# Kernel tuning notes

Measured on AMD Instinct MI355X. Metric: run time of the kernel, lower is better.

The kernel has to match this reference:

```python
import jax, jax.numpy as jnp
import numpy as np

DIM = 256
NUM_HEADS = 8
HEAD_DIM = DIM // NUM_HEADS
SCALE = HEAD_DIM ** -0.5
KSIZE = 5


def setup_inputs() -> dict:
    key = jax.random.key(0)
    ks = jax.random.split(key, 6)
    B, C, H, W = 8, DIM, 32, 32
    x = jax.random.normal(ks[0], (B, C, H, W), dtype=jnp.float32)
    qkv_w = jax.random.normal(ks[1], (3 * C, C), dtype=jnp.float32) * 0.02  # 1x1 conv, no bias
    proj_w = jax.random.normal(ks[2], (C, C), dtype=jnp.float32) * 0.02    # 1x1 conv
    proj_b = jax.random.normal(ks[3], (C,), dtype=jnp.float32) * 0.02
    lepe_w = jax.random.normal(ks[4], (C, 1, KSIZE, KSIZE), dtype=jnp.float32) * 0.02  # depthwise
    lepe_b = jax.random.normal(ks[5], (C,), dtype=jnp.float32) * 0.02
    return {"x": x, "qkv_w": qkv_w, "proj_w": proj_w, "proj_b": proj_b,
            "lepe_w": lepe_w, "lepe_b": lepe_b}


def _forward(x, qkv_w, proj_w, proj_b, lepe_w, lepe_b):
    B, C, H, W = x.shape
    N = H * W
    # 1x1 conv qkv: [B,3C,H,W]
    qkv = jnp.einsum('bchw,oc->bohw', x, qkv_w)
    q, k, v = jnp.split(qkv, 3, axis=1)
    # reshape to [B, heads, head_dim, N]
    qh = q.reshape(B, NUM_HEADS, HEAD_DIM, N)
    kh = k.reshape(B, NUM_HEADS, HEAD_DIM, N)
    vh = v.reshape(B, NUM_HEADS, HEAD_DIM, N)
    # attn = (q^T k) * scale, softmax over keys -> [B, heads, N, N]
    attn = jnp.einsum('bhdn,bhdm->bhnm', qh, kh)
    attn = jax.nn.softmax(attn * SCALE, axis=-1)
    # out = attn @ v^T -> [B, heads, N, head_dim] -> [B, C, H, W]
    out = jnp.einsum('bhnm,bhdm->bhdn', attn, vh).reshape(B, C, H, W)
    # LePE: depthwise conv on v (image layout) + residual add
    lepe = jax.lax.conv_general_dilated(
        v, lepe_w, window_strides=(1, 1),
        padding=[(KSIZE // 2, KSIZE // 2)] * 2,
        dimension_numbers=('NCHW', 'OIHW', 'NCHW'),
        feature_group_count=C) + lepe_b[None, :, None, None]
    out = out + lepe
    # 1x1 proj
    out = jnp.einsum('bchw,oc->bohw', out, proj_w) + proj_b[None, :, None, None]
    return out


def reference(x, qkv_w, proj_w, proj_b, lepe_w, lepe_b):
    return _forward(x, qkv_w, proj_w, proj_b, lepe_w, lepe_b)
```

## Files before the change

kernel.cpp:

```cpp
#include <hip/hip_runtime.h>

#define NB 8
#define NC 256
#define NN 1024

typedef unsigned short u16;
typedef unsigned int u32;
typedef __attribute__((ext_vector_type(8))) short short8;
typedef __attribute__((ext_vector_type(4))) float f32x4;

__device__ __forceinline__ u16 f2b(float f){ union{float ff;u32 i;}v; v.ff=f; u32 r=v.i+0x7FFFu+((v.i>>16)&1u); return (u16)(r>>16); }
__device__ __forceinline__ float b2f(u16 p){ union{u32 i;float f;}v; v.i=((u32)p)<<16; return v.f; }
__device__ __forceinline__ float pklo(u32 p){ union{u32 i;float f;}v; v.i=p<<16; return v.f; }
__device__ __forceinline__ float pkhi(u32 p){ union{u32 i;float f;}v; v.i=p&0xFFFF0000u; return v.f; }

#define QSC 0.25503486f

union FR { uint4 u; short8 s; };

__global__ void __launch_bounds__(256) k_cast(const float* __restrict__ qkvw,
                                              const float* __restrict__ projw,
                                              const float* __restrict__ x,
                                              u16* __restrict__ wb,
                                              u16* __restrict__ xt){
  __shared__ u16 lt[64][136];
  const int tid = threadIdx.x;
  if (blockIdx.x < 256){
    const int idx = blockIdx.x*256 + tid;
    const float* src = (idx < 49152) ? (qkvw + (size_t)idx*4)
                                     : (projw + (size_t)(idx-49152)*4);
    float4 a = *(const float4*)src;
    uint2 o;
    o.x = (u32)f2b(a.x) | ((u32)f2b(a.y)<<16);
    o.y = (u32)f2b(a.z) | ((u32)f2b(a.w)<<16);
    *(uint2*)(wb + (size_t)idx*4) = o;
    return;
  }
  const int bx = blockIdx.x - 256;
  const int n0 = (bx & 15)*64, c0 = ((bx>>4)&1)*128, b = bx>>5;
  #pragma unroll
  for (int cc = 0; cc < 4; cc++){
    const int c = c0 + cc*32 + (tid>>3);
    const int ns = (tid&7)*8;
    const float* src = x + ((size_t)(b*NC + c))*NN + n0 + ns;
    float4 a = *(const float4*)src;
    float4 d = *(const float4*)(src+4);
    const int cl = c - c0;
    lt[ns+0][cl] = f2b(a.x); lt[ns+1][cl] = f2b(a.y);
    lt[ns+2][cl] = f2b(a.z); lt[ns+3][cl] = f2b(a.w);
    lt[ns+4][cl] = f2b(d.x); lt[ns+5][cl] = f2b(d.y);
    lt[ns+6][cl] = f2b(d.z); lt[ns+7][cl] = f2b(d.w);
  }
  __syncthreads();
  #pragma unroll
  for (int p = 0; p < 4; p++){
    const int flat = p*256 + tid;
    const int row = flat >> 4, seg = flat & 15;
    uint4 d = *(uint4*)&lt[row][seg*8];
    *(uint4*)(xt + ((size_t)(b*NN + n0 + row))*NC + c0 + seg*8) = d;
  }
}

__global__ void __launch_bounds__(256) k_qkv(const u16* __restrict__ wqb,
                                             const u16* __restrict__ xt,
                                             u16* __restrict__ qt,
                                             u16* __restrict__ kt,
                                             u16* __restrict__ v){
  const int ot = blockIdx.x, nt = blockIdx.y, b = blockIdx.z;
  const int o0 = ot*32;
  const int tid = threadIdx.x, wv = tid>>6, lane = tid&63;
  const int l15 = lane&15, quad = lane>>4;
  const int n0w = nt*256 + wv*64;
  __shared__ u16 swq[32][264];
  __shared__ u16 s2[4][64][40];
  #pragma unroll
  for (int i = 0; i < 4; i++){
    const int flat = i*256 + tid;
    const int row = flat >> 5, col = flat & 31;
    *(uint4*)&swq[row][col*8] = *(const uint4*)(wqb + (size_t)(o0+row)*NC + col*8);
  }
  __syncthreads();
  f32x4 acc[2][4];
  #pragma unroll
  for (int mt = 0; mt < 2; mt++)
    #pragma unroll
    for (int nt2 = 0; nt2 < 4; nt2++) acc[mt][nt2] = (f32x4){0.f,0.f,0.f,0.f};
  const u16* xb = xt + ((size_t)(b*NN + n0w))*NC;
  for (int k0 = 0; k0 < 256; k0 += 32){
    FR af[2], bf[4];
    af[0].u = *(uint4*)&swq[l15][k0 + quad*8];
    af[1].u = *(uint4*)&swq[16+l15][k0 + quad*8];
    #pragma unroll
    for (int nt2 = 0; nt2 < 4; nt2++)
      bf[nt2].u = *(const uint4*)(xb + (size_t)(nt2*16+l15)*NC + k0 + quad*8);
    #pragma unroll
    for (int mt = 0; mt < 2; mt++)
      #pragma unroll
      for (int nt2 = 0; nt2 < 4; nt2++)
        acc[mt][nt2] = __builtin_amdgcn_mfma_f32_16x16x32_bf16(af[mt].s, bf[nt2].s, acc[mt][nt2], 0,0,0);
  }
  if (ot < 16){
    const float sc = (ot < 8) ? QSC : 1.0f;
    u16* dstbase = (ot < 8) ? qt : kt;
    const int h = (ot < 8) ? ot : ot-8;
    #pragma unroll
    for (int mt = 0; mt < 2; mt++)
      #pragma unroll
      for (int nt2 = 0; nt2 < 4; nt2++){
        uint2 w;
        w.x = (u32)f2b(acc[mt][nt2][0]*sc) | ((u32)f2b(acc[mt][nt2][1]*sc)<<16);
        w.y = (u32)f2b(acc[mt][nt2][2]*sc) | ((u32)f2b(acc[mt][nt2][3]*sc)<<16);
        *(uint2*)&s2[wv][nt2*16+l15][mt*16+quad*4] = w;
      }
    __syncthreads();
    u16* db = dstbase + ((size_t)(b*8+h)*NN + n0w)*32;
    #pragma unroll
    for (int p = 0; p < 4; p++){
      const int n_loc = p*16 + (lane>>2), seg = lane&3;
      uint4 d = *(uint4*)&s2[wv][n_loc][seg*8];
      *(uint4*)(db + (size_t)n_loc*32 + seg*8) = d;
    }
  } else {
    const int c0 = o0 - 512;
    #pragma unroll
    for (int mt = 0; mt < 2; mt++)
      #pragma unroll
      for (int nt2 = 0; nt2 < 4; nt2++)
        #pragma unroll
        for (int r = 0; r < 4; r++)
          v[(size_t)(b*NC + c0 + mt*16 + quad*4 + r)*NN + n0w + nt2*16 + l15] = f2b(acc[mt][nt2][r]);
  }
}

__global__ void __launch_bounds__(256) k_attn(const u16* __restrict__ qt,
                                              const u16* __restrict__ kt,
                                              const u16* __restrict__ v,
                                              const float* __restrict__ lw,
                                              const float* __restrict__ lb,
                                              u16* __restrict__ tt){
  const int h = blockIdx.y, b = blockIdx.z;
  const int tid = threadIdx.x;
  const int wv = tid >> 6, lane = tid & 63;
  const int l15 = lane & 15, quad = lane >> 4;
  const int bh = b*8 + h;
  const int q0 = (blockIdx.x*4 + wv)*32;

  __shared__ u16 pb[4][2][16][40];
  __shared__ u16 vstage[8][32][38];
  __shared__ u16 s_out[4][32][36];
  u16* pbA = &pb[wv][0][0][0];
  u16* pbB = &pb[wv][1][0][0];

  {
    const int rr = tid >> 5, lc2 = tid & 31;
    const int yy = blockIdx.x*4 - 2 + rr;
    u32* dst32 = (u32*)&vstage[rr][lc2][0];
    if (yy < 0 || yy > 31){
      #pragma unroll
      for (int j = 0; j < 19; j++) dst32[j] = 0;
    } else {
      const u16* src = v + ((size_t)(b*NC + h*32 + lc2))*NN + yy*32;
      uint4 a = *(const uint4*)src;
      uint4 b4 = *(const uint4*)(src+8);
      uint4 c4 = *(const uint4*)(src+16);
      uint4 d4 = *(const uint4*)(src+24);
      dst32[0] = 0;
      dst32[1]=a.x;  dst32[2]=a.y;  dst32[3]=a.z;  dst32[4]=a.w;
      dst32[5]=b4.x; dst32[6]=b4.y; dst32[7]=b4.z; dst32[8]=b4.w;
      dst32[9]=c4.x; dst32[10]=c4.y; dst32[11]=c4.z; dst32[12]=c4.w;
      dst32[13]=d4.x; dst32[14]=d4.y; dst32[15]=d4.z; dst32[16]=d4.w;
      dst32[17]=0; dst32[18]=0;
    }
  }
  __syncthreads();

  const u16* qtb = qt + (size_t)bh*NN*32;
  const u16* ktb = kt + (size_t)bh*NN*32;
  const u16* vbp = v + (size_t)(b*256 + h*32)*NN;

  FR qa, qb_;
  qa.u  = *(const uint4*)(qtb + (size_t)(q0      + l15)*32 + quad*8);
  qb_.u = *(const uint4*)(qtb + (size_t)(q0 + 16 + l15)*32 + quad*8);

  f32x4 z = {0.f,0.f,0.f,0.f};
  f32x4 oA0 = z, oA1 = z, oB0 = z, oB1 = z;
  float denA[4] = {0.f,0.f,0.f,0.f}, denB[4] = {0.f,0.f,0.f,0.f};

  for (int m0 = 0; m0 < NN; m0 += 32){
    FR kf0, kf1, vf0, vf1;
    kf0.u = *(const uint4*)(ktb + (size_t)(m0      + l15)*32 + quad*8);
    kf1.u = *(const uint4*)(ktb + (size_t)(m0 + 16 + l15)*32 + quad*8);
    vf0.u = *(const uint4*)(vbp + (size_t)(l15     )*NN + m0 + quad*8);
    vf1.u = *(const uint4*)(vbp + (size_t)(16 + l15)*NN + m0 + quad*8);

    f32x4 sA0 = __builtin_amdgcn_mfma_f32_16x16x32_bf16(qa.s,  kf0.s, z, 0,0,0);
    f32x4 sA1 = __builtin_amdgcn_mfma_f32_16x16x32_bf16(qa.s,  kf1.s, z, 0,0,0);
    f32x4 sB0 = __builtin_amdgcn_mfma_f32_16x16x32_bf16(qb_.s, kf0.s, z, 0,0,0);
    f32x4 sB1 = __builtin_amdgcn_mfma_f32_16x16x32_bf16(qb_.s, kf1.s, z, 0,0,0);

    #pragma unroll
    for (int r = 0; r < 4; r++){
      float pA0 = __builtin_amdgcn_exp2f(sA0[r]);
      float pA1 = __builtin_amdgcn_exp2f(sA1[r]);
      float pB0 = __builtin_amdgcn_exp2f(sB0[r]);
      float pB1 = __builtin_amdgcn_exp2f(sB1[r]);
      denA[r] += pA0 + pA1;
      denB[r] += pB0 + pB1;
      const int row = (quad*4 + r)*40;
      pbA[row + l15]      = (u16)(__float_as_uint(pA0)>>16);
      pbA[row + 16 + l15] = (u16)(__float_as_uint(pA1)>>16);
      pbB[row + l15]      = (u16)(__float_as_uint(pB0)>>16);
      pbB[row + 16 + l15] = (u16)(__float_as_uint(pB1)>>16);
    }
    FR pfA, pfB;
    pfA.u = *(const uint4*)(pbA + l15*40 + quad*8);
    pfB.u = *(const uint4*)(pbB + l15*40 + quad*8);

    oA0 = __builtin_amdgcn_mfma_f32_16x16x32_bf16(pfA.s, vf0.s, oA0, 0,0,0);
    oA1 = __builtin_amdgcn_mfma_f32_16x16x32_bf16(pfA.s, vf1.s, oA1, 0,0,0);
    oB0 = __builtin_amdgcn_mfma_f32_16x16x32_bf16(pfB.s, vf0.s, oB0, 0,0,0);
    oB1 = __builtin_amdgcn_mfma_f32_16x16x32_bf16(pfB.s, vf1.s, oB1, 0,0,0);
  }
  #pragma unroll
  for (int r = 0; r < 4; r++){
    #pragma unroll
    for (int m = 1; m < 16; m <<= 1){
      denA[r] += __shfl_xor(denA[r], m);
      denB[r] += __shfl_xor(denB[r], m);
    }
  }
  {
    u16* so = &s_out[wv][0][0];
    #pragma unroll
    for (int r = 0; r < 4; r++){
      const int q = quad*4 + r;
      const float iA = 1.f/denA[r], iB = 1.f/denB[r];
      so[q*36 + l15]           = f2b(oA0[r]*iA);
      so[q*36 + 16 + l15]      = f2b(oA1[r]*iA);
      so[(q+16)*36 + l15]      = f2b(oB0[r]*iB);
      so[(q+16)*36 + 16 + l15] = f2b(oB1[r]*iB);
    }
  }
  {
    const int lc = lane & 31, qh = lane >> 5;
    float lep[16];
    const float lbias = lb[h*32 + lc];
    #pragma unroll
    for (int i = 0; i < 16; i++) lep[i] = lbias;
    const float* lwc = lw + (size_t)(h*32 + lc)*25;
    #pragma unroll
    for (int ky = 0; ky < 5; ky++){
      const u32* vr = (const u32*)&vstage[wv + ky][lc][0];
      float vv[20];
      #pragma unroll
      for (int jj = 0; jj < 10; jj++){
        u32 pk = vr[qh*8 + jj];
        vv[2*jj]   = pklo(pk);
        vv[2*jj+1] = pkhi(pk);
      }
      const float w0 = lwc[ky*5+0], w1 = lwc[ky*5+1], w2 = lwc[ky*5+2],
                  w3 = lwc[ky*5+3], w4 = lwc[ky*5+4];
      #pragma unroll
      for (int i = 0; i < 16; i++)
        lep[i] += w0*vv[i] + w1*vv[i+1] + w2*vv[i+2] + w3*vv[i+3] + w4*vv[i+4];
    }
    u16* tb = tt + ((size_t)(b*NN + q0))*NC + h*32;
    const u16* so = &s_out[wv][0][0];
    #pragma unroll
    for (int i = 0; i < 16; i++){
      const int q = qh*16 + i;
      tb[(size_t)q*NC + lc] = f2b(b2f(so[q*36 + lc]) + lep[i]);
    }
  }
}

__global__ void __launch_bounds__(256) k_proj(const u16* __restrict__ wpb,
                                              const u16* __restrict__ tt,
                                              const float* __restrict__ pbias,
                                              float* __restrict__ out){
  const int ot = blockIdx.x, nt = blockIdx.y, b = blockIdx.z;
  const int o0 = ot*32;
  const int tid = threadIdx.x, wv = tid>>6, lane = tid&63;
  const int l15 = lane&15, quad = lane>>4;
  const int n0w = nt*256 + wv*64;
  __shared__ u16 swp[32][264];
  #pragma unroll
  for (int i = 0; i < 4; i++){
    const int flat = i*256 + tid;
    const int row = flat >> 5, col = flat & 31;
    *(uint4*)&swp[row][col*8] = *(const uint4*)(wpb + (size_t)(o0+row)*NC + col*8);
  }
  __syncthreads();
  f32x4 acc[2][4];
  #pragma unroll
  for (int mt = 0; mt < 2; mt++)
    #pragma unroll
    for (int nt2 = 0; nt2 < 4; nt2++) acc[mt][nt2] = (f32x4){0.f,0.f,0.f,0.f};
  const u16* tb = tt + ((size_t)(b*NN + n0w))*NC;
  for (int k0 = 0; k0 < 256; k0 += 32){
    FR af[2], bf[4];
    af[0].u = *(uint4*)&swp[l15][k0 + quad*8];
    af[1].u = *(uint4*)&swp[16+l15][k0 + quad*8];
    #pragma unroll
    for (int nt2 = 0; nt2 < 4; nt2++)
      bf[nt2].u = *(const uint4*)(tb + (size_t)(nt2*16+l15)*NC + k0 + quad*8);
    #pragma unroll
    for (int mt = 0; mt < 2; mt++)
      #pragma unroll
      for (int nt2 = 0; nt2 < 4; nt2++)
        acc[mt][nt2] = __builtin_amdgcn_mfma_f32_16x16x32_bf16(af[mt].s, bf[nt2].s, acc[mt][nt2], 0,0,0);
  }
  float bv[2][4];
  #pragma unroll
  for (int mt = 0; mt < 2; mt++)
    #pragma unroll
    for (int r = 0; r < 4; r++) bv[mt][r] = pbias[o0 + mt*16 + quad*4 + r];
  #pragma unroll
  for (int mt = 0; mt < 2; mt++)
    #pragma unroll
    for (int nt2 = 0; nt2 < 4; nt2++)
      #pragma unroll
      for (int r = 0; r < 4; r++)
        out[(size_t)(b*NC + o0 + mt*16 + quad*4 + r)*NN + n0w + nt2*16 + l15] = acc[mt][nt2][r] + bv[mt][r];
}

extern "C" void kernel_launch(void* const* d_in, const int* in_sizes, int n_in,
                              void* d_out, int out_size, void* d_ws, size_t ws_size,
                              hipStream_t stream){
  const float* x      = (const float*)d_in[0];
  const float* qkv_w  = (const float*)d_in[1];
  const float* proj_w = (const float*)d_in[2];
  const float* proj_b = (const float*)d_in[3];
  const float* lepe_w = (const float*)d_in[4];
  const float* lepe_b = (const float*)d_in[5];
  float* out = (float*)d_out;

  if (ws_size < (size_t)21495808) return;
  u16* wqb = (u16*)d_ws;
  u16* wpb = wqb + 196608;
  u16* xt  = wpb + 65536;
  u16* qt  = xt + 2097152;
  u16* kt  = qt + 2097152;
  u16* v   = kt + 2097152;
  u16* tt  = v  + 2097152;

  k_cast<<<dim3(512),     256, 0, stream>>>(qkv_w, proj_w, x, wqb, xt);
  k_qkv <<<dim3(24, 4, 8),256, 0, stream>>>(wqb, xt, qt, kt, v);
  k_attn<<<dim3(8, 8, 8), 256, 0, stream>>>(qt, kt, v, lepe_w, lepe_b, tt);
  k_proj<<<dim3(8, 4, 8), 256, 0, stream>>>(wpb, tt, proj_b, out);
}
```

Before: 121.5 us.

## Fuse attention, LePE and output projection into one kernel per query tile

```diff
diff --git a/kernel.cpp b/kernel.cpp
--- a/kernel.cpp
+++ b/kernel.cpp
@@ -132,34 +132,36 @@
   }
 }
 
-__global__ void __launch_bounds__(256) k_attn(const u16* __restrict__ qt,
-                                              const u16* __restrict__ kt,
-                                              const u16* __restrict__ v,
-                                              const float* __restrict__ lw,
-                                              const float* __restrict__ lb,
-                                              u16* __restrict__ tt){
-  const int h = blockIdx.y, b = blockIdx.z;
+__global__ void __launch_bounds__(512) k_attn_proj(const u16* __restrict__ qt,
+                                                   const u16* __restrict__ kt,
+                                                   const u16* __restrict__ v,
+                                                   const float* __restrict__ lw,
+                                                   const float* __restrict__ lb,
+                                                   const u16* __restrict__ wpb,
+                                                   const float* __restrict__ pbias,
+                                                   float* __restrict__ out){
+  const int b = blockIdx.x, y = blockIdx.y;
   const int tid = threadIdx.x;
   const int wv = tid >> 6, lane = tid & 63;
   const int l15 = lane & 15, quad = lane >> 4;
-  const int bh = b*8 + h;
-  const int q0 = (blockIdx.x*4 + wv)*32;
-
-  __shared__ u16 pb[4][2][16][40];
-  __shared__ u16 vstage[8][32][38];
-  __shared__ u16 s_out[4][32][36];
+  const int h = wv, bh = b*8 + h;
+  const int q0 = y*32;
+
+  __shared__ u16 pb[8][2][16][40];
+  __shared__ u16 vstage[5][256][38];
+  __shared__ u16 s_out[32][264];
   u16* pbA = &pb[wv][0][0][0];
   u16* pbB = &pb[wv][1][0][0];
 
-  {
-    const int rr = tid >> 5, lc2 = tid & 31;
-    const int yy = blockIdx.x*4 - 2 + rr;
-    u32* dst32 = (u32*)&vstage[rr][lc2][0];
+  for (int p = tid; p < 1280; p += 512){
+    const int rr = p >> 8, c = p & 255;
+    const int yy = y - 2 + rr;
+    u32* dst32 = (u32*)&vstage[rr][c][0];
     if (yy < 0 || yy > 31){
       #pragma unroll
       for (int j = 0; j < 19; j++) dst32[j] = 0;
     } else {
-      const u16* src = v + ((size_t)(b*NC + h*32 + lc2))*NN + yy*32;
+      const u16* src = v + ((size_t)(b*NC + c))*NN + yy*32;
       uint4 a = *(const uint4*)src;
       uint4 b4 = *(const uint4*)(src+8);
       uint4 c4 = *(const uint4*)(src+16);
@@ -230,15 +232,15 @@
     }
   }
   {
-    u16* so = &s_out[wv][0][0];
+    const int cb = wv*32;
     #pragma unroll
     for (int r = 0; r < 4; r++){
       const int q = quad*4 + r;
       const float iA = 1.f/denA[r], iB = 1.f/denB[r];
-      so[q*36 + l15]           = f2b(oA0[r]*iA);
-      so[q*36 + 16 + l15]      = f2b(oA1[r]*iA);
-      so[(q+16)*36 + l15]      = f2b(oB0[r]*iB);
-      so[(q+16)*36 + 16 + l15] = f2b(oB1[r]*iB);
+      s_out[q][cb + l15]           = f2b(oA0[r]*iA);
+      s_out[q][cb + 16 + l15]      = f2b(oA1[r]*iA);
+      s_out[q+16][cb + l15]        = f2b(oB0[r]*iB);
+      s_out[q+16][cb + 16 + l15]   = f2b(oB1[r]*iB);
     }
   }
   {
@@ -250,7 +252,7 @@
     const float* lwc = lw + (size_t)(h*32 + lc)*25;
     #pragma unroll
     for (int ky = 0; ky < 5; ky++){
-      const u32* vr = (const u32*)&vstage[wv + ky][lc][0];
+      const u32* vr = (const u32*)&vstage[ky][wv*32 + lc][0];
       float vv[20];
       #pragma unroll
       for (int jj = 0; jj < 10; jj++){
@@ -264,64 +266,47 @@
       for (int i = 0; i < 16; i++)
         lep[i] += w0*vv[i] + w1*vv[i+1] + w2*vv[i+2] + w3*vv[i+3] + w4*vv[i+4];
     }
-    u16* tb = tt + ((size_t)(b*NN + q0))*NC + h*32;
-    const u16* so = &s_out[wv][0][0];
     #pragma unroll
     for (int i = 0; i < 16; i++){
       const int q = qh*16 + i;
-      tb[(size_t)q*NC + lc] = f2b(b2f(so[q*36 + lc]) + lep[i]);
-    }
-  }
-}
-
-__global__ void __launch_bounds__(256) k_proj(const u16* __restrict__ wpb,
-                                              const u16* __restrict__ tt,
-                                              const float* __restrict__ pbias,
-                                              float* __restrict__ out){
-  const int ot = blockIdx.x, nt = blockIdx.y, b = blockIdx.z;
-  const int o0 = ot*32;
-  const int tid = threadIdx.x, wv = tid>>6, lane = tid&63;
-  const int l15 = lane&15, quad = lane>>4;
-  const int n0w = nt*256 + wv*64;
-  __shared__ u16 swp[32][264];
-  #pragma unroll
-  for (int i = 0; i < 4; i++){
-    const int flat = i*256 + tid;
-    const int row = flat >> 5, col = flat & 31;
-    *(uint4*)&swp[row][col*8] = *(const uint4*)(wpb + (size_t)(o0+row)*NC + col*8);
+      u16* p = &s_out[q][wv*32 + lc];
+      *p = f2b(b2f(*p) + lep[i]);
+    }
   }
   __syncthreads();
-  f32x4 acc[2][4];
-  #pragma unroll
-  for (int mt = 0; mt < 2; mt++)
-    #pragma unroll
-    for (int nt2 = 0; nt2 < 4; nt2++) acc[mt][nt2] = (f32x4){0.f,0.f,0.f,0.f};
-  const u16* tb = tt + ((size_t)(b*NN + n0w))*NC;
-  for (int k0 = 0; k0 < 256; k0 += 32){
-    FR af[2], bf[4];
-    af[0].u = *(uint4*)&swp[l15][k0 + quad*8];
-    af[1].u = *(uint4*)&swp[16+l15][k0 + quad*8];
-    #pragma unroll
-    for (int nt2 = 0; nt2 < 4; nt2++)
-      bf[nt2].u = *(const uint4*)(tb + (size_t)(nt2*16+l15)*NC + k0 + quad*8);
-    #pragma unroll
-    for (int mt = 0; mt < 2; mt++)
-      #pragma unroll
-      for (int nt2 = 0; nt2 < 4; nt2++)
-        acc[mt][nt2] = __builtin_amdgcn_mfma_f32_16x16x32_bf16(af[mt].s, bf[nt2].s, acc[mt][nt2], 0,0,0);
-  }
-  float bv[2][4];
-  #pragma unroll
-  for (int mt = 0; mt < 2; mt++)
-    #pragma unroll
-    for (int r = 0; r < 4; r++) bv[mt][r] = pbias[o0 + mt*16 + quad*4 + r];
-  #pragma unroll
-  for (int mt = 0; mt < 2; mt++)
-    #pragma unroll
-    for (int nt2 = 0; nt2 < 4; nt2++)
-      #pragma unroll
-      for (int r = 0; r < 4; r++)
-        out[(size_t)(b*NC + o0 + mt*16 + quad*4 + r)*NN + n0w + nt2*16 + l15] = acc[mt][nt2][r] + bv[mt][r];
+
+  {
+    const int o0 = wv*32;
+    f32x4 accp[2][2];
+    #pragma unroll
+    for (int mt = 0; mt < 2; mt++)
+      #pragma unroll
+      for (int nt2 = 0; nt2 < 2; nt2++) accp[mt][nt2] = (f32x4){0.f,0.f,0.f,0.f};
+    for (int k0 = 0; k0 < 256; k0 += 32){
+      FR af[2], bf2[2];
+      af[0].u = *(const uint4*)(wpb + (size_t)(o0 + l15)*NC + k0 + quad*8);
+      af[1].u = *(const uint4*)(wpb + (size_t)(o0 + 16 + l15)*NC + k0 + quad*8);
+      bf2[0].u = *(const uint4*)&s_out[l15][k0 + quad*8];
+      bf2[1].u = *(const uint4*)&s_out[16 + l15][k0 + quad*8];
+      #pragma unroll
+      for (int mt = 0; mt < 2; mt++)
+        #pragma unroll
+        for (int nt2 = 0; nt2 < 2; nt2++)
+          accp[mt][nt2] = __builtin_amdgcn_mfma_f32_16x16x32_bf16(af[mt].s, bf2[nt2].s, accp[mt][nt2], 0,0,0);
+    }
+    float bv[2][4];
+    #pragma unroll
+    for (int mt = 0; mt < 2; mt++)
+      #pragma unroll
+      for (int r = 0; r < 4; r++) bv[mt][r] = pbias[o0 + mt*16 + quad*4 + r];
+    #pragma unroll
+    for (int mt = 0; mt < 2; mt++)
+      #pragma unroll
+      for (int nt2 = 0; nt2 < 2; nt2++)
+        #pragma unroll
+        for (int r = 0; r < 4; r++)
+          out[(size_t)(b*NC + o0 + mt*16 + quad*4 + r)*NN + y*32 + nt2*16 + l15] = accp[mt][nt2][r] + bv[mt][r];
+  }
 }
 
 extern "C" void kernel_launch(void* const* d_in, const int* in_sizes, int n_in,
@@ -335,17 +320,15 @@
   const float* lepe_b = (const float*)d_in[5];
   float* out = (float*)d_out;
 
-  if (ws_size < (size_t)21495808) return;
+  if (ws_size < (size_t)17301504) return;
   u16* wqb = (u16*)d_ws;
   u16* wpb = wqb + 196608;
   u16* xt  = wpb + 65536;
   u16* qt  = xt + 2097152;
   u16* kt  = qt + 2097152;
   u16* v   = kt + 2097152;
-  u16* tt  = v  + 2097152;
-
-  k_cast<<<dim3(512),     256, 0, stream>>>(qkv_w, proj_w, x, wqb, xt);
-  k_qkv <<<dim3(24, 4, 8),256, 0, stream>>>(wqb, xt, qt, kt, v);
-  k_attn<<<dim3(8, 8, 8), 256, 0, stream>>>(qt, kt, v, lepe_w, lepe_b, tt);
-  k_proj<<<dim3(8, 4, 8), 256, 0, stream>>>(wpb, tt, proj_b, out);
+
+  k_cast<<<dim3(512),      256, 0, stream>>>(qkv_w, proj_w, x, wqb, xt);
+  k_qkv <<<dim3(24, 4, 8), 256, 0, stream>>>(wqb, xt, qt, kt, v);
+  k_attn_proj<<<dim3(8, 32), 512, 0, stream>>>(qt, kt, v, lepe_w, lepe_b, wpb, proj_b, out);
 }
```

Result: no change. 122.2 us (+0.6%).
